# Kernel tuning notes

Hardware: AMD Instinct MI355X
Metric: run time of the kernel (lower is better)

Reference implementation:

```python
import jax, jax.numpy as jnp
import numpy as np

BIAS = 7  # FP8 E4M3 exponent bias


def _decode(bits):
    # bits [..., 8] in order [s, e3, e2, e1, e0, m2, m1, m0]
    b = bits.astype(jnp.int32)
    s = b[..., 0]
    e = (b[..., 1] << 3) | (b[..., 2] << 2) | (b[..., 3] << 1) | b[..., 4]
    m = (b[..., 5] << 2) | (b[..., 6] << 1) | b[..., 7]
    return s, e, m


def _rne_rshift(M, sh):
    # round-to-nearest-even right shift of non-negative int M by sh (sh >= 0)
    q = M >> sh
    rem = M - (q << sh)
    half = jnp.right_shift(jnp.left_shift(1, sh), 1)  # 2^(sh-1), 0 when sh==0
    up = ((rem > half) | ((rem == half) & ((q & 1) == 1))) & (sh > 0)
    return q + up.astype(jnp.int32)


def setup_inputs() -> dict:
    key = jax.random.key(0)
    ks = jax.random.split(key, 6)
    shape = (1024, 4096)

    def make(k1, k2, k3):
        s = jax.random.randint(k1, shape, 0, 2)
        e = jax.random.randint(k2, shape, 0, 15)  # exclude e=15 (NaN region) for well-defined inputs
        m = jax.random.randint(k3, shape, 0, 8)
        bits = jnp.stack([s, (e >> 3) & 1, (e >> 2) & 1, (e >> 1) & 1, e & 1,
                          (m >> 2) & 1, (m >> 1) & 1, m & 1], axis=-1)
        return bits.astype(jnp.float32)

    return {"a": make(ks[0], ks[1], ks[2]), "b": make(ks[3], ks[4], ks[5])}


def _fp8_mul(a, b):
    sa, ea, ma = _decode(a)
    sb, eb_, mb = _decode(b)
    # significand with implicit bit; subnormals (e==0) use leading-zero-normalized form,
    # identical math to the module's mux_a_leading / shift_calc path
    sig_a = jnp.where(ea == 0, ma, ma + 8)
    sig_b = jnp.where(eb_ == 0, mb, mb + 8)
    exa = jnp.where(ea == 0, 1, ea) - BIAS
    exb = jnp.where(eb_ == 0, 1, eb_) - BIAS
    M = sig_a * sig_b              # exact 8-bit product, <= 225 (the 4x4 array multiplier)
    E = exa + exb - 6              # value = M * 2^E  (each sig in units of 2^-3)
    # MSB position p of M (M in [1, 225] => p in [0, 7])
    p = sum(((M >= (1 << k)).astype(jnp.int32) for k in range(1, 8)), start=jnp.zeros_like(M))
    eb_out = E + p + BIAS          # candidate biased exponent (normalization unit)
    # ---- normal path (eb_out >= 1): RNE round to 3 mantissa bits ----
    sh = p - 3
    shp = jnp.maximum(sh, 0)
    lsh = jnp.maximum(-sh, 0)
    mant4 = jnp.left_shift(_rne_rshift(M, shp), lsh)  # in [8, 16]
    carry = mant4 >> 4                                # rounding overflow -> exp += 1
    mant4 = jnp.where(mant4 == 16, 8, mant4)
    e_n = eb_out + carry
    m_n = mant4 - 8
    nan = e_n >= 16                                   # exponent overflow -> NaN (e=1111, m=111)
    e_n = jnp.where(nan, 15, e_n)
    m_n = jnp.where(nan, 7, m_n)
    # ---- subnormal path (eb_out <= 0): mant = RNE(M * 2^(E+9)), value = mant * 2^-9 ----
    t = E + 9
    mant_s = jnp.left_shift(_rne_rshift(M, jnp.clip(-t, 0, 30)), jnp.maximum(t, 0))
    e_s = jnp.where(mant_s >= 8, 1, 0)                # rounding promoted to smallest normal
    m_s = jnp.where(mant_s >= 8, 0, mant_s)
    # ---- select ----
    is_sub = eb_out <= 0
    e_o = jnp.where(is_sub, e_s, e_n)
    m_o = jnp.where(is_sub, m_s, m_n)
    zero = M == 0                                     # either input true zero
    e_o = jnp.where(zero, 0, e_o)
    m_o = jnp.where(zero, 0, m_o)
    s_o = sa ^ sb
    bits = jnp.stack([s_o, (e_o >> 3) & 1, (e_o >> 2) & 1, (e_o >> 1) & 1, e_o & 1,
                      (m_o >> 2) & 1, (m_o >> 1) & 1, m_o & 1], axis=-1)
    return bits.astype(jnp.float32)


def reference(a, b):
    return _fp8_mul(a, b)
```

## Files before the change

### kernel.cpp

```cpp
#include <hip/hip_runtime.h>


#define BIAS 7
#define G 2

typedef unsigned int u32x4 __attribute__((ext_vector_type(4)));

__device__ __forceinline__ int rne_rshift(int M, int sh) {
    int q = M >> sh;
    int rem = M - (q << sh);
    int half = (1 << sh) >> 1;
    int up = ((rem > half) | ((rem == half) & (q & 1))) & (sh > 0);
    return q + up;
}

__device__ __forceinline__ int fp8_mul_group(u32x4 a0, u32x4 a1, u32x4 b0, u32x4 b1) {
    int sa = (a0.x >> 23) & 1;
    int ea = ((a0.y >> 20) & 8) | ((a0.z >> 21) & 4) | ((a0.w >> 22) & 2) | ((a1.x >> 23) & 1);
    int ma = ((a1.y >> 21) & 4) | ((a1.z >> 22) & 2) | ((a1.w >> 23) & 1);
    int sb = (b0.x >> 23) & 1;
    int eb = ((b0.y >> 20) & 8) | ((b0.z >> 21) & 4) | ((b0.w >> 22) & 2) | ((b1.x >> 23) & 1);
    int mb = ((b1.y >> 21) & 4) | ((b1.z >> 22) & 2) | ((b1.w >> 23) & 1);

    int sig_a = (ea == 0) ? ma : (ma + 8);
    int sig_b = (eb == 0) ? mb : (mb + 8);
    int exa = ((ea == 0) ? 1 : ea) - BIAS;
    int exb = ((eb == 0) ? 1 : eb) - BIAS;

    int M = sig_a * sig_b;
    int E = exa + exb - 6;

    int p = (M > 0) ? (31 - __clz(M)) : 0;
    int eb_out = E + p + BIAS;

    int sh  = p - 3;
    int shp = (sh > 0) ? sh : 0;
    int lsh = (sh < 0) ? -sh : 0;
    int mant4 = rne_rshift(M, shp) << lsh;
    int carry = mant4 >> 4;
    if (mant4 == 16) mant4 = 8;
    int e_n = eb_out + carry;
    int m_n = mant4 - 8;
    if (e_n >= 16) { e_n = 15; m_n = 7; }

    int t = E + 9;
    int rsh   = (-t < 0) ? 0 : ((-t > 30) ? 30 : -t);
    int lsh_s = (t > 0) ? t : 0;
    int mant_s = rne_rshift(M, rsh) << lsh_s;
    int e_s = (mant_s >= 8) ? 1 : 0;
    int m_s = (mant_s >= 8) ? 0 : mant_s;

    int is_sub = (eb_out <= 0);
    int e_o = is_sub ? e_s : e_n;
    int m_o = is_sub ? m_s : m_n;
    if (M == 0) { e_o = 0; m_o = 0; }
    int s_o = sa ^ sb;
    return (s_o << 7) | (e_o << 3) | m_o;
}

__global__ void __launch_bounds__(256)
fp8_mul_kernel(const u32x4* __restrict__ a, const u32x4* __restrict__ b,
               u32x4* __restrict__ out, int n_groups) {
    int base = (blockIdx.x * blockDim.x + threadIdx.x) * G;
    if (base >= n_groups) return;

    u32x4 av[2 * G], bv[2 * G];
#pragma unroll
    for (int g = 0; g < 2 * G; ++g) av[g] = a[2 * base + g];
#pragma unroll
    for (int g = 0; g < 2 * G; ++g) bv[g] = b[2 * base + g];

    const unsigned ONE = 0x3F800000u;
#pragma unroll
    for (int g = 0; g < G; ++g) {
        int r = fp8_mul_group(av[2 * g], av[2 * g + 1], bv[2 * g], bv[2 * g + 1]);
        u32x4 o0, o1;
        o0.x = (r & 0x80) ? ONE : 0u;
        o0.y = (r & 0x40) ? ONE : 0u;
        o0.z = (r & 0x20) ? ONE : 0u;
        o0.w = (r & 0x10) ? ONE : 0u;
        o1.x = (r & 0x08) ? ONE : 0u;
        o1.y = (r & 0x04) ? ONE : 0u;
        o1.z = (r & 0x02) ? ONE : 0u;
        o1.w = (r & 0x01) ? ONE : 0u;
        out[2 * (base + g)]     = o0;
        out[2 * (base + g) + 1] = o1;
    }
}

extern "C" void kernel_launch(void* const* d_in, const int* in_sizes, int n_in,
                              void* d_out, int out_size, void* d_ws, size_t ws_size,
                              hipStream_t stream) {
    const u32x4* a = (const u32x4*)d_in[0];
    const u32x4* b = (const u32x4*)d_in[1];
    u32x4* out = (u32x4*)d_out;
    int n_groups = in_sizes[0] / 8;
    int threads = (n_groups + G - 1) / G;
    int block = 256;
    int grid = (threads + block - 1) / block;
    fp8_mul_kernel<<<grid, block, 0, stream>>>(a, b, out, n_groups);
}
```

Before: 311.2 us.

## Switch to grid-stride loop with software-prefetched next group

Replaces the fixed two-groups-per-thread mapping with a persistent grid-stride loop over a capped grid of 2048 blocks. Each iteration issues the loads for the next group before computing and storing the current one, so memory latency overlaps with the decode and multiply logic. The fixed grid means fewer threads in flight, so bandwidth saturation now depends on the prefetch depth of one group per thread.

```diff
diff --git a/kernel.cpp b/kernel.cpp
--- a/kernel.cpp
+++ b/kernel.cpp
@@ -2,7 +2,6 @@
 
 
 #define BIAS 7
-#define G 2
 
 typedef unsigned int u32x4 __attribute__((ext_vector_type(4)));
 
@@ -58,33 +57,44 @@
     return (s_o << 7) | (e_o << 3) | m_o;
 }
 
+__device__ __forceinline__ void emit(u32x4* __restrict__ out, int g, int r) {
+    const unsigned ONE = 0x3F800000u;
+    u32x4 o0, o1;
+    o0.x = (r & 0x80) ? ONE : 0u;
+    o0.y = (r & 0x40) ? ONE : 0u;
+    o0.z = (r & 0x20) ? ONE : 0u;
+    o0.w = (r & 0x10) ? ONE : 0u;
+    o1.x = (r & 0x08) ? ONE : 0u;
+    o1.y = (r & 0x04) ? ONE : 0u;
+    o1.z = (r & 0x02) ? ONE : 0u;
+    o1.w = (r & 0x01) ? ONE : 0u;
+    out[2 * g]     = o0;
+    out[2 * g + 1] = o1;
+}
+
 __global__ void __launch_bounds__(256)
 fp8_mul_kernel(const u32x4* __restrict__ a, const u32x4* __restrict__ b,
                u32x4* __restrict__ out, int n_groups) {
-    int base = (blockIdx.x * blockDim.x + threadIdx.x) * G;
-    if (base >= n_groups) return;
+    int nt = gridDim.x * blockDim.x;
+    int g  = blockIdx.x * blockDim.x + threadIdx.x;
+    if (g >= n_groups) return;
 
-    u32x4 av[2 * G], bv[2 * G];
-#pragma unroll
-    for (int g = 0; g < 2 * G; ++g) av[g] = a[2 * base + g];
-#pragma unroll
-    for (int g = 0; g < 2 * G; ++g) bv[g] = b[2 * base + g];
+    u32x4 a0 = a[2 * g], a1 = a[2 * g + 1];
+    u32x4 b0 = b[2 * g], b1 = b[2 * g + 1];
 
-    const unsigned ONE = 0x3F800000u;
-#pragma unroll
-    for (int g = 0; g < G; ++g) {
-        int r = fp8_mul_group(av[2 * g], av[2 * g + 1], bv[2 * g], bv[2 * g + 1]);
-        u32x4 o0, o1;
-        o0.x = (r & 0x80) ? ONE : 0u;
-        o0.y = (r & 0x40) ? ONE : 0u;
-        o0.z = (r & 0x20) ? ONE : 0u;
-        o0.w = (r & 0x10) ? ONE : 0u;
-        o1.x = (r & 0x08) ? ONE : 0u;
-        o1.y = (r & 0x04) ? ONE : 0u;
-        o1.z = (r & 0x02) ? ONE : 0u;
-        o1.w = (r & 0x01) ? ONE : 0u;
-        out[2 * (base + g)]     = o0;
-        out[2 * (base + g) + 1] = o1;
+    while (true) {
+        int gn = g + nt;
+        u32x4 na0, na1, nb0, nb1;
+        bool more = gn < n_groups;
+        if (more) {
+            na0 = a[2 * gn]; na1 = a[2 * gn + 1];
+            nb0 = b[2 * gn]; nb1 = b[2 * gn + 1];
+        }
+        int r = fp8_mul_group(a0, a1, b0, b1);
+        emit(out, g, r);
+        if (!more) break;
+        g = gn;
+        a0 = na0; a1 = na1; b0 = nb0; b1 = nb1;
     }
 }
 
@@ -95,8 +105,9 @@
     const u32x4* b = (const u32x4*)d_in[1];
     u32x4* out = (u32x4*)d_out;
     int n_groups = in_sizes[0] / 8;
-    int threads = (n_groups + G - 1) / G;
     int block = 256;
-    int grid = (threads + block - 1) / block;
+    int grid = 2048;
+    int max_grid = (n_groups + block - 1) / block;
+    if (grid > max_grid) grid = max_grid;
     fp8_mul_kernel<<<grid, block, 0, stream>>>(a, b, out, n_groups);
 }
```

Result: no change. 313.0 us (+0.6%).
